# Optimization experiments

Hardware: AMD Instinct MI355X
Metric: run time of the kernel (lower is better)

Reference implementation:

```python
import jax, jax.numpy as jnp
import numpy as np

N_NODES = 50000
N_EDGES = 800000
IN_SIZE, HID_SIZE, OUT_SIZE = 512, 128, 64


def _graph_conv(feat, src, dst, W, b, out_norm, in_norm, activation=None):
    # DGL GraphConv with norm='both': h' = D_in^{-1/2} A D_out^{-1/2} (X W) + b
    x = feat * out_norm[:, None]          # scale by source (out-degree) norm
    x = x @ W                             # dense transform first (in >= out)
    msg = x[src]                          # gather per-edge messages [E, d]
    agg = jax.ops.segment_sum(msg, dst, num_segments=N_NODES)
    h = agg * in_norm[:, None] + b
    if activation is not None:
        h = activation(h)
    return h


def setup_inputs() -> dict:
    key = jax.random.key(0)
    k1, k2, k3, k4, k5, k6, k7 = jax.random.split(key, 7)
    features = jax.random.normal(k1, (N_NODES, IN_SIZE), dtype=jnp.float32)
    src = jax.random.randint(k2, (N_EDGES,), 0, N_NODES, dtype=jnp.int64)
    dst = jax.random.randint(k3, (N_EDGES,), 0, N_NODES, dtype=jnp.int64)
    # Glorot-style init as in dglnn.GraphConv
    W1 = jax.random.normal(k4, (IN_SIZE, HID_SIZE), dtype=jnp.float32) * (1.0 / np.sqrt(IN_SIZE))
    b1 = jnp.zeros((HID_SIZE,), dtype=jnp.float32)
    W2 = jax.random.normal(k5, (HID_SIZE, OUT_SIZE), dtype=jnp.float32) * (1.0 / np.sqrt(HID_SIZE))
    b2 = jnp.zeros((OUT_SIZE,), dtype=jnp.float32)
    return {"features": features, "W1": W1, "b1": b1, "W2": W2, "b2": b2,
            "src": src, "dst": dst}


def reference(features, W1, b1, W2, b2, src, dst):
    ones = jnp.ones((N_EDGES,), dtype=features.dtype)
    out_deg = jax.ops.segment_sum(ones, src, num_segments=N_NODES)
    in_deg = jax.ops.segment_sum(ones, dst, num_segments=N_NODES)
    out_norm = jax.lax.rsqrt(jnp.clip(out_deg, 1.0))  # deg clamped to >=1 as in DGL
    in_norm = jax.lax.rsqrt(jnp.clip(in_deg, 1.0))
    h = _graph_conv(features, src, dst, W1, b1, out_norm, in_norm, activation=jax.nn.relu)
    # dropout omitted (eval mode)
    h = _graph_conv(h, src, dst, W2, b2, out_norm, in_norm, activation=None)
    return h
```

## Files before the change

kernel.cpp:

```cpp
#include <hip/hip_runtime.h>

#define N_NODES 50000
#define IN_SIZE 512
#define HID 128
#define OUT 64
#define NB 256
#define SHIFT 7
#define NBUCK 391
#define NBINS8 12500

typedef _Float16 f16x8 __attribute__((ext_vector_type(8)));
typedef _Float16 f16x4 __attribute__((ext_vector_type(4)));
typedef float    f32x4 __attribute__((ext_vector_type(4)));

__device__ __forceinline__ bool detect_w(const int* p, int t, int* sh) {
    if (t < 64) {
        unsigned long long m = __ballot(p[2 * t + 1] == 0);
        if (t == 0) *sh = (m == ~0ull) ? 1 : 0;
    }
    __syncthreads();
    return *sh != 0;
}

__device__ __forceinline__ int load_idx(const void* p, int e, bool w) {
    return w ? (int)((const long long*)p)[e] : ((const int*)p)[e];
}

__global__ __launch_bounds__(256) void k_hist_wt(const void* __restrict__ srcp,
                                                 const void* __restrict__ dstp,
                                                 int* __restrict__ hist,
                                                 unsigned int* __restrict__ spart,
                                                 int E, int EPB,
                                                 const float* __restrict__ W1, _Float16* __restrict__ W1T,
                                                 const float* __restrict__ W2, _Float16* __restrict__ W2T) {
    const int t = threadIdx.x, b = blockIdx.x;
    if (b >= NB) {
        int i = (b - NB) * 256 + t;
        if (i < IN_SIZE * HID) {
            int k = i >> 7, n = i & (HID - 1);
            W1T[(size_t)n * IN_SIZE + k] = (_Float16)W1[i];
        } else {
            int j = i - IN_SIZE * HID;
            if (j < HID * OUT) {
                int k = j >> 6, n = j & (OUT - 1);
                W2T[(size_t)n * HID + k] = (_Float16)W2[j];
            }
        }
        return;
    }
    __shared__ unsigned int sbins[NBINS8];
    __shared__ int dbins[NBUCK];
    __shared__ int shw;
    for (int i = t; i < NBINS8; i += 256) sbins[i] = 0;
    for (int i = t; i < NBUCK; i += 256) dbins[i] = 0;
    bool w = detect_w((const int*)dstp, t, &shw);
    __syncthreads();
    int eend = min(E, (b + 1) * EPB);
    for (int e = b * EPB + t; e < eend; e += 256) {
        int s = load_idx(srcp, e, w);
        int d = load_idx(dstp, e, w);
        atomicAdd(&dbins[d >> SHIFT], 1);
        atomicAdd(&sbins[s >> 2], 1u << ((s & 3) << 3));
    }
    __syncthreads();
    for (int i = t; i < NBUCK; i += 256) hist[i * NB + b] = dbins[i];
    for (int i = t; i < NBINS8; i += 256) spart[(size_t)b * NBINS8 + i] = sbins[i];
}

__global__ __launch_bounds__(256) void k_scanA(int* __restrict__ hist, int* __restrict__ bsum) {
    __shared__ int s[256];
    const int t = threadIdx.x, g = blockIdx.x;
    int v = hist[g * NB + t];
    s[t] = v;
    __syncthreads();
    for (int off = 1; off < 256; off <<= 1) {
        int u = (t >= off) ? s[t - off] : 0;
        __syncthreads();
        s[t] += u;
        __syncthreads();
    }
    hist[g * NB + t] = s[t] - v;
    if (t == 255) bsum[g] = s[255];
}

__global__ __launch_bounds__(512) void k_scanB(const int* __restrict__ bsum, int* __restrict__ bb) {
    __shared__ int s[512];
    const int t = threadIdx.x;
    int v = (t < NBUCK) ? bsum[t] : 0;
    s[t] = v;
    __syncthreads();
    for (int off = 1; off < 512; off <<= 1) {
        int u = (t >= off) ? s[t - off] : 0;
        __syncthreads();
        s[t] += u;
        __syncthreads();
    }
    if (t <= NBUCK) bb[t] = s[t] - v;
}

__global__ __launch_bounds__(256) void k_cscatter(const void* __restrict__ srcp,
                                                  const void* __restrict__ dstp,
                                                  const int* __restrict__ hist,
                                                  const int* __restrict__ bb,
                                                  unsigned int* __restrict__ tmp,
                                                  int E, int EPB) {
    __shared__ int cur[NBUCK];
    __shared__ int shw;
    const int t = threadIdx.x, b = blockIdx.x;
    for (int i = t; i < NBUCK; i += 256) cur[i] = hist[i * NB + b] + bb[i];
    bool w = detect_w((const int*)dstp, t, &shw);
    __syncthreads();
    int eend = min(E, (b + 1) * EPB);
    for (int e = b * EPB + t; e < eend; e += 256) {
        int s = load_idx(srcp, e, w);
        int d = load_idx(dstp, e, w);
        int pos = atomicAdd(&cur[d >> SHIFT], 1);
        tmp[pos] = (unsigned int)s | ((unsigned int)(d & 127) << 16);
    }
}

__global__ __launch_bounds__(256) void k_fine(const unsigned int* __restrict__ tmp,
                                              const int* __restrict__ bb,
                                              const unsigned int* __restrict__ partial,
                                              int* __restrict__ rp,
                                              int* __restrict__ esrc,
                                              float* __restrict__ innorm,
                                              float* __restrict__ onorm) {
    __shared__ int fcnt[128];
    __shared__ int sc[128];
    __shared__ int fcur[128];
    __shared__ int rs[256][4];
    const int t = threadIdx.x, u = blockIdx.x;
    const int e0 = bb[u], e1 = bb[u + 1];
    if (t < 128) fcnt[t] = 0;
    __syncthreads();
    for (int e = e0 + t; e < e1; e += 256)
        atomicAdd(&fcnt[tmp[e] >> 16], 1);
    {
        const int wrd = t & 31, grp = t >> 5;
        const int wd = u * 32 + wrd;
        int c0 = 0, c1 = 0, c2 = 0, c3 = 0;
        if (wd < NBINS8) {
            for (int b = grp * 32; b < grp * 32 + 32; ++b) {
                unsigned int v = partial[(size_t)b * NBINS8 + wd];
                c0 += (int)(v & 255u);
                c1 += (int)((v >> 8) & 255u);
                c2 += (int)((v >> 16) & 255u);
                c3 += (int)(v >> 24);
            }
        }
        rs[t][0] = c0; rs[t][1] = c1; rs[t][2] = c2; rs[t][3] = c3;
    }
    __syncthreads();
    if (t < 32) {
        const int wd = u * 32 + t;
        if (wd < NBINS8) {
            int d0 = 0, d1 = 0, d2 = 0, d3 = 0;
            for (int g = 0; g < 8; ++g) {
                d0 += rs[g * 32 + t][0]; d1 += rs[g * 32 + t][1];
                d2 += rs[g * 32 + t][2]; d3 += rs[g * 32 + t][3];
            }
            if (d0 < 1) d0 = 1; if (d1 < 1) d1 = 1;
            if (d2 < 1) d2 = 1; if (d3 < 1) d3 = 1;
            int n0 = 4 * wd;
            if (n0     < N_NODES) onorm[n0]     = 1.0f / sqrtf((float)d0);
            if (n0 + 1 < N_NODES) onorm[n0 + 1] = 1.0f / sqrtf((float)d1);
            if (n0 + 2 < N_NODES) onorm[n0 + 2] = 1.0f / sqrtf((float)d2);
            if (n0 + 3 < N_NODES) onorm[n0 + 3] = 1.0f / sqrtf((float)d3);
        }
    }
    if (t < 128) sc[t] = fcnt[t];
    __syncthreads();
    for (int off = 1; off < 128; off <<= 1) {
        int v = (t < 128 && t >= off) ? sc[t - off] : 0;
        __syncthreads();
        if (t < 128) sc[t] += v;
        __syncthreads();
    }
    if (t < 128) {
        int base = e0 + sc[t] - fcnt[t];
        fcur[t] = base;
        int node = u * 128 + t;
        if (node < N_NODES) {
            rp[node] = base;
            int c = fcnt[t]; if (c < 1) c = 1;
            innorm[node] = 1.0f / sqrtf((float)c);
        }
    }
    if (u == NBUCK - 1 && t == 0) rp[N_NODES] = e1;
    __syncthreads();
    for (int e = e0 + t; e < e1; e += 256) {
        unsigned int p = tmp[e];
        int pos = atomicAdd(&fcur[p >> 16], 1);
        esrc[pos] = (int)(p & 0xFFFFu);
    }
}

#define LDA 44
__global__ __launch_bounds__(256) void k_gemm1_mfma(const float* __restrict__ A,
                                                    const _Float16* __restrict__ BT,
                                                    const float* __restrict__ onorm,
                                                    _Float16* __restrict__ X) {
    __shared__ _Float16 As[2][64 * LDA];
    __shared__ _Float16 Bs[2][64 * LDA];
    const int tid  = threadIdx.x;
    const int wave = tid >> 6, lane = tid & 63;
    const int lm = lane & 15, lq = lane >> 4;
    const int row0 = (blockIdx.x >> 1) * 64;
    const int ch   = (blockIdx.x & 1) * 64;

    const int ar = tid >> 2, aq = tid & 3;
    int arow = row0 + ar; if (arow >= N_NODES) arow = N_NODES - 1;
    const float* aptr = A + (size_t)arow * IN_SIZE + aq * 8;
    const int bn = tid >> 2, bq = tid & 3;
    const _Float16* bptr = BT + (size_t)(ch + bn) * IN_SIZE + bq * 8;

    f32x4 acc[4];
#pragma unroll
    for (int nt = 0; nt < 4; ++nt) acc[nt] = (f32x4){0.f, 0.f, 0.f, 0.f};

    {
        float4 a0 = *(const float4*)(aptr);
        float4 a1 = *(const float4*)(aptr + 4);
        f16x8  b0 = *(const f16x8*)(bptr);
        f16x8 ap = {(_Float16)a0.x, (_Float16)a0.y, (_Float16)a0.z, (_Float16)a0.w,
                    (_Float16)a1.x, (_Float16)a1.y, (_Float16)a1.z, (_Float16)a1.w};
        *(f16x8*)&As[0][ar * LDA + aq * 8] = ap;
        *(f16x8*)&Bs[0][bn * LDA + bq * 8] = b0;
    }
    __syncthreads();

#pragma unroll
    for (int kt = 0; kt < IN_SIZE / 32; ++kt) {
        const int k0 = kt * 32;
        const int cur = kt & 1;
        float4 na0, na1; f16x8 nb0;
        const bool more = (k0 + 32) < IN_SIZE;
        if (more) {
            na0 = *(const float4*)(aptr + k0 + 32);
            na1 = *(const float4*)(aptr + k0 + 36);
            nb0 = *(const f16x8*)(bptr + k0 + 32);
        }
        f16x8 af = *(const f16x8*)&As[cur][(wave * 16 + lm) * LDA + lq * 8];
#pragma unroll
        for (int nt = 0; nt < 4; ++nt) {
            f16x8 bf = *(const f16x8*)&Bs[cur][(nt * 16 + lm) * LDA + lq * 8];
            acc[nt] = __builtin_amdgcn_mfma_f32_16x16x32_f16(af, bf, acc[nt], 0, 0, 0);
        }
        if (more) {
            f16x8 ap = {(_Float16)na0.x, (_Float16)na0.y, (_Float16)na0.z, (_Float16)na0.w,
                        (_Float16)na1.x, (_Float16)na1.y, (_Float16)na1.z, (_Float16)na1.w};
            *(f16x8*)&As[cur ^ 1][ar * LDA + aq * 8] = ap;
            *(f16x8*)&Bs[cur ^ 1][bn * LDA + bq * 8] = nb0;
            __syncthreads();
        }
    }
#pragma unroll
    for (int i = 0; i < 4; ++i) {
        int row = row0 + wave * 16 + lq * 4 + i;
        if (row < N_NODES) {
            float on = onorm[row];
            _Float16* o = X + (size_t)row * HID + ch + lm;
#pragma unroll
            for (int nt = 0; nt < 4; ++nt)
                o[nt * 16] = (_Float16)(acc[nt][i] * on);
        }
    }
}

#define LDH 136
__global__ __launch_bounds__(256) void k_agg1_fused(const _Float16* __restrict__ X, const int* __restrict__ rp,
                                                    const int* __restrict__ esrc, const float* __restrict__ innorm,
                                                    const float* __restrict__ onorm, const float* __restrict__ b1,
                                                    const _Float16* __restrict__ W2T, _Float16* __restrict__ X2) {
    __shared__ _Float16 Hs[16 * LDH];
    const int t = threadIdx.x;
    const int ln = t >> 4;
    const int c  = (t & 15) << 3;
    const int n  = blockIdx.x * 16 + ln;
    const int e0 = rp[n], e1 = rp[n + 1];
    float a[8] = {0.f, 0.f, 0.f, 0.f, 0.f, 0.f, 0.f, 0.f};
    int e = e0;
    for (; e + 3 < e1; e += 4) {
        int s0 = esrc[e], s1 = esrc[e + 1], s2 = esrc[e + 2], s3 = esrc[e + 3];
        f16x8 v0 = *(const f16x8*)&X[(size_t)s0 * HID + c];
        f16x8 v1 = *(const f16x8*)&X[(size_t)s1 * HID + c];
        f16x8 v2 = *(const f16x8*)&X[(size_t)s2 * HID + c];
        f16x8 v3 = *(const f16x8*)&X[(size_t)s3 * HID + c];
#pragma unroll
        for (int j = 0; j < 8; ++j)
            a[j] += ((float)v0[j] + (float)v1[j]) + ((float)v2[j] + (float)v3[j]);
    }
    for (; e < e1; ++e) {
        f16x8 v = *(const f16x8*)&X[(size_t)esrc[e] * HID + c];
#pragma unroll
        for (int j = 0; j < 8; ++j) a[j] += (float)v[j];
    }
    const float inn = innorm[n], on = onorm[n];
    float4 bA = *(const float4*)&b1[c];
    float4 bB = *(const float4*)&b1[c + 4];
    const float bv[8] = {bA.x, bA.y, bA.z, bA.w, bB.x, bB.y, bB.z, bB.w};
    f16x8 h;
#pragma unroll
    for (int j = 0; j < 8; ++j)
        h[j] = (_Float16)(fmaxf(a[j] * inn + bv[j], 0.f) * on);
    *(f16x8*)&Hs[ln * LDH + c] = h;
    __syncthreads();

    const int wave = t >> 6, lane = t & 63;
    const int lm = lane & 15, lq = lane >> 4;
    f32x4 acc = (f32x4){0.f, 0.f, 0.f, 0.f};
#pragma unroll
    for (int k0 = 0; k0 < HID; k0 += 32) {
        f16x8 af = *(const f16x8*)&Hs[lm * LDH + k0 + lq * 8];
        f16x8 bf = *(const f16x8*)&W2T[(size_t)(wave * 16 + lm) * HID + k0 + lq * 8];
        acc = __builtin_amdgcn_mfma_f32_16x16x32_f16(af, bf, acc, 0, 0, 0);
    }
    const int n0 = blockIdx.x * 16;
#pragma unroll
    for (int i = 0; i < 4; ++i) {
        int row = n0 + lq * 4 + i;
        X2[(size_t)row * OUT + wave * 16 + lm] = (_Float16)acc[i];
    }
}

__global__ __launch_bounds__(256) void k_agg2(const _Float16* __restrict__ X2, const int* __restrict__ rp,
                                              const int* __restrict__ esrc, const float* __restrict__ innorm,
                                              const float* __restrict__ b2, float* __restrict__ out) {
    const int n = blockIdx.x * 32 + (threadIdx.x >> 3);
    const int c = (threadIdx.x & 7) << 3;
    if (n >= N_NODES) return;
    const int e0 = rp[n], e1 = rp[n + 1];
    float a[8] = {0.f, 0.f, 0.f, 0.f, 0.f, 0.f, 0.f, 0.f};
    int e = e0;
    for (; e + 3 < e1; e += 4) {
        int s0 = esrc[e], s1 = esrc[e + 1], s2 = esrc[e + 2], s3 = esrc[e + 3];
        f16x8 v0 = *(const f16x8*)&X2[(size_t)s0 * OUT + c];
        f16x8 v1 = *(const f16x8*)&X2[(size_t)s1 * OUT + c];
        f16x8 v2 = *(const f16x8*)&X2[(size_t)s2 * OUT + c];
        f16x8 v3 = *(const f16x8*)&X2[(size_t)s3 * OUT + c];
#pragma unroll
        for (int j = 0; j < 8; ++j)
            a[j] += ((float)v0[j] + (float)v1[j]) + ((float)v2[j] + (float)v3[j]);
    }
    for (; e < e1; ++e) {
        f16x8 v = *(const f16x8*)&X2[(size_t)esrc[e] * OUT + c];
#pragma unroll
        for (int j = 0; j < 8; ++j) a[j] += (float)v[j];
    }
    const float inn = innorm[n];
    float4 bA = *(const float4*)&b2[c];
    float4 bB = *(const float4*)&b2[c + 4];
    float* o = out + (size_t)n * OUT + c;
    *(float4*)o       = make_float4(a[0] * inn + bA.x, a[1] * inn + bA.y,
                                    a[2] * inn + bA.z, a[3] * inn + bA.w);
    *(float4*)(o + 4) = make_float4(a[4] * inn + bB.x, a[5] * inn + bB.y,
                                    a[6] * inn + bB.z, a[7] * inn + bB.w);
}

extern "C" void kernel_launch(void* const* d_in, const int* in_sizes, int n_in,
                              void* d_out, int out_size, void* d_ws, size_t ws_size,
                              hipStream_t stream) {
    const float* feat = (const float*)d_in[0];
    const float* W1   = (const float*)d_in[1];
    const float* b1   = (const float*)d_in[2];
    const float* W2   = (const float*)d_in[3];
    const float* b2   = (const float*)d_in[4];
    const void*  srcp = (const void*)d_in[5];
    const void*  dstp = (const void*)d_in[6];
    const int    E    = in_sizes[5];
    float* out = (float*)d_out;

    char* w = (char*)d_ws;
    size_t off = 0;
    auto alloc = [&](size_t bytes) -> void* {
        off = (off + 255) & ~(size_t)255;
        void* p = w + off;
        off += bytes;
        return p;
    };
    int*   hist    = (int*)alloc((size_t)NBUCK * NB * 4);
    int*   bsum    = (int*)alloc((size_t)NBUCK * 4);
    int*   bb      = (int*)alloc((size_t)(NBUCK + 1) * 4);
    int*   rp      = (int*)alloc((size_t)(N_NODES + 1) * 4);
    unsigned int* spart = (unsigned int*)alloc((size_t)NB * NBINS8 * 4);
    unsigned int* tmp   = (unsigned int*)alloc((size_t)E * 4);
    int*   esrc    = (int*)alloc((size_t)E * 4);
    float* onorm   = (float*)alloc((size_t)N_NODES * 4);
    float* innorm  = (float*)alloc((size_t)N_NODES * 4);
    _Float16* W1T  = (_Float16*)alloc((size_t)IN_SIZE * HID * 2);
    _Float16* W2T  = (_Float16*)alloc((size_t)HID * OUT * 2);
    _Float16* X1   = (_Float16*)alloc((size_t)N_NODES * HID * 2);
    _Float16* X2   = (_Float16*)alloc((size_t)N_NODES * OUT * 2);
    (void)ws_size; (void)n_in; (void)out_size;

    const int EPB = (E + NB - 1) / NB;
    const int WTB = (IN_SIZE * HID + HID * OUT + 255) / 256;

    k_hist_wt<<<NB + WTB, 256, 0, stream>>>(srcp, dstp, hist, spart, E, EPB, W1, W1T, W2, W2T);
    k_scanA<<<NBUCK, 256, 0, stream>>>(hist, bsum);
    k_scanB<<<1, 512, 0, stream>>>(bsum, bb);
    k_cscatter<<<NB, 256, 0, stream>>>(srcp, dstp, hist, bb, tmp, E, EPB);
    k_fine<<<NBUCK, 256, 0, stream>>>(tmp, bb, spart, rp, esrc, innorm, onorm);

    k_gemm1_mfma<<<((N_NODES + 63) / 64) * 2, 256, 0, stream>>>(feat, W1T, onorm, X1);
    k_agg1_fused<<<(N_NODES + 15) / 16, 256, 0, stream>>>(X1, rp, esrc, innorm, onorm, b1, W2T, X2);
    k_agg2<<<(N_NODES + 31) / 32, 256, 0, stream>>>(X2, rp, esrc, innorm, b2, out);
}
```

Before: 273.1 us.

## Replace per-block shared out-degree histograms with global atomics; unroll gathers to 8

Out-degree counting moves from per-block packed 8-bit shared-memory histograms (written to a 256x12500 partial buffer and reduced in k_fine) to direct global atomicAdd on a 50000-entry counter, zeroed by a new small kernel. This removes about 12.8 MB of partial writes and reads plus the large shared-memory allocation in the histogram kernel, which should raise its occupancy. In exchange it adds 800K global atomics and an extra launch. Separately, both aggregation kernels unroll the edge gather loop from 4 to 8 to keep more loads in flight.

```diff
diff --git a/kernel.cpp b/kernel.cpp
--- a/kernel.cpp
+++ b/kernel.cpp
@@ -7,7 +7,6 @@
 #define NB 256
 #define SHIFT 7
 #define NBUCK 391
-#define NBINS8 12500
 
 typedef _Float16 f16x8 __attribute__((ext_vector_type(8)));
 typedef _Float16 f16x4 __attribute__((ext_vector_type(4)));
@@ -26,10 +25,15 @@
     return w ? (int)((const long long*)p)[e] : ((const int*)p)[e];
 }
 
+__global__ __launch_bounds__(256) void k_zero(unsigned int* __restrict__ outdeg) {
+    int i = blockIdx.x * 256 + threadIdx.x;
+    if (i < N_NODES) outdeg[i] = 0u;
+}
+
 __global__ __launch_bounds__(256) void k_hist_wt(const void* __restrict__ srcp,
                                                  const void* __restrict__ dstp,
                                                  int* __restrict__ hist,
-                                                 unsigned int* __restrict__ spart,
+                                                 unsigned int* __restrict__ outdeg,
                                                  int E, int EPB,
                                                  const float* __restrict__ W1, _Float16* __restrict__ W1T,
                                                  const float* __restrict__ W2, _Float16* __restrict__ W2T) {
@@ -48,10 +52,8 @@
         }
         return;
     }
-    __shared__ unsigned int sbins[NBINS8];
     __shared__ int dbins[NBUCK];
     __shared__ int shw;
-    for (int i = t; i < NBINS8; i += 256) sbins[i] = 0;
     for (int i = t; i < NBUCK; i += 256) dbins[i] = 0;
     bool w = detect_w((const int*)dstp, t, &shw);
     __syncthreads();
@@ -60,11 +62,10 @@
         int s = load_idx(srcp, e, w);
         int d = load_idx(dstp, e, w);
         atomicAdd(&dbins[d >> SHIFT], 1);
-        atomicAdd(&sbins[s >> 2], 1u << ((s & 3) << 3));
+        atomicAdd(&outdeg[s], 1u);
     }
     __syncthreads();
     for (int i = t; i < NBUCK; i += 256) hist[i * NB + b] = dbins[i];
-    for (int i = t; i < NBINS8; i += 256) spart[(size_t)b * NBINS8 + i] = sbins[i];
 }
 
 __global__ __launch_bounds__(256) void k_scanA(int* __restrict__ hist, int* __restrict__ bsum) {
@@ -121,7 +122,7 @@
 
 __global__ __launch_bounds__(256) void k_fine(const unsigned int* __restrict__ tmp,
                                               const int* __restrict__ bb,
-                                              const unsigned int* __restrict__ partial,
+                                              const unsigned int* __restrict__ outdeg,
                                               int* __restrict__ rp,
                                               int* __restrict__ esrc,
                                               float* __restrict__ innorm,
@@ -129,46 +130,13 @@
     __shared__ int fcnt[128];
     __shared__ int sc[128];
     __shared__ int fcur[128];
-    __shared__ int rs[256][4];
     const int t = threadIdx.x, u = blockIdx.x;
     const int e0 = bb[u], e1 = bb[u + 1];
     if (t < 128) fcnt[t] = 0;
     __syncthreads();
     for (int e = e0 + t; e < e1; e += 256)
         atomicAdd(&fcnt[tmp[e] >> 16], 1);
-    {
-        const int wrd = t & 31, grp = t >> 5;
-        const int wd = u * 32 + wrd;
-        int c0 = 0, c1 = 0, c2 = 0, c3 = 0;
-        if (wd < NBINS8) {
-            for (int b = grp * 32; b < grp * 32 + 32; ++b) {
-                unsigned int v = partial[(size_t)b * NBINS8 + wd];
-                c0 += (int)(v & 255u);
-                c1 += (int)((v >> 8) & 255u);
-                c2 += (int)((v >> 16) & 255u);
-                c3 += (int)(v >> 24);
-            }
-        }
-        rs[t][0] = c0; rs[t][1] = c1; rs[t][2] = c2; rs[t][3] = c3;
-    }
-    __syncthreads();
-    if (t < 32) {
-        const int wd = u * 32 + t;
-        if (wd < NBINS8) {
-            int d0 = 0, d1 = 0, d2 = 0, d3 = 0;
-            for (int g = 0; g < 8; ++g) {
-                d0 += rs[g * 32 + t][0]; d1 += rs[g * 32 + t][1];
-                d2 += rs[g * 32 + t][2]; d3 += rs[g * 32 + t][3];
-            }
-            if (d0 < 1) d0 = 1; if (d1 < 1) d1 = 1;
-            if (d2 < 1) d2 = 1; if (d3 < 1) d3 = 1;
-            int n0 = 4 * wd;
-            if (n0     < N_NODES) onorm[n0]     = 1.0f / sqrtf((float)d0);
-            if (n0 + 1 < N_NODES) onorm[n0 + 1] = 1.0f / sqrtf((float)d1);
-            if (n0 + 2 < N_NODES) onorm[n0 + 2] = 1.0f / sqrtf((float)d2);
-            if (n0 + 3 < N_NODES) onorm[n0 + 3] = 1.0f / sqrtf((float)d3);
-        }
-    }
+    __syncthreads();
     if (t < 128) sc[t] = fcnt[t];
     __syncthreads();
     for (int off = 1; off < 128; off <<= 1) {
@@ -185,6 +153,8 @@
             rp[node] = base;
             int c = fcnt[t]; if (c < 1) c = 1;
             innorm[node] = 1.0f / sqrtf((float)c);
+            unsigned int od = outdeg[node]; if (od < 1u) od = 1u;
+            onorm[node] = 1.0f / sqrtf((float)od);
         }
     }
     if (u == NBUCK - 1 && t == 0) rp[N_NODES] = e1;
@@ -281,15 +251,19 @@
     const int e0 = rp[n], e1 = rp[n + 1];
     float a[8] = {0.f, 0.f, 0.f, 0.f, 0.f, 0.f, 0.f, 0.f};
     int e = e0;
-    for (; e + 3 < e1; e += 4) {
-        int s0 = esrc[e], s1 = esrc[e + 1], s2 = esrc[e + 2], s3 = esrc[e + 3];
-        f16x8 v0 = *(const f16x8*)&X[(size_t)s0 * HID + c];
-        f16x8 v1 = *(const f16x8*)&X[(size_t)s1 * HID + c];
-        f16x8 v2 = *(const f16x8*)&X[(size_t)s2 * HID + c];
-        f16x8 v3 = *(const f16x8*)&X[(size_t)s3 * HID + c];
+    for (; e + 7 < e1; e += 8) {
+        f16x8 v0 = *(const f16x8*)&X[(size_t)esrc[e]     * HID + c];
+        f16x8 v1 = *(const f16x8*)&X[(size_t)esrc[e + 1] * HID + c];
+        f16x8 v2 = *(const f16x8*)&X[(size_t)esrc[e + 2] * HID + c];
+        f16x8 v3 = *(const f16x8*)&X[(size_t)esrc[e + 3] * HID + c];
+        f16x8 v4 = *(const f16x8*)&X[(size_t)esrc[e + 4] * HID + c];
+        f16x8 v5 = *(const f16x8*)&X[(size_t)esrc[e + 5] * HID + c];
+        f16x8 v6 = *(const f16x8*)&X[(size_t)esrc[e + 6] * HID + c];
+        f16x8 v7 = *(const f16x8*)&X[(size_t)esrc[e + 7] * HID + c];
 #pragma unroll
         for (int j = 0; j < 8; ++j)
-            a[j] += ((float)v0[j] + (float)v1[j]) + ((float)v2[j] + (float)v3[j]);
+            a[j] += (((float)v0[j] + (float)v1[j]) + ((float)v2[j] + (float)v3[j])) +
+                    (((float)v4[j] + (float)v5[j]) + ((float)v6[j] + (float)v7[j]));
     }
     for (; e < e1; ++e) {
         f16x8 v = *(const f16x8*)&X[(size_t)esrc[e] * HID + c];
@@ -333,15 +307,19 @@
     const int e0 = rp[n], e1 = rp[n + 1];
     float a[8] = {0.f, 0.f, 0.f, 0.f, 0.f, 0.f, 0.f, 0.f};
     int e = e0;
-    for (; e + 3 < e1; e += 4) {
-        int s0 = esrc[e], s1 = esrc[e + 1], s2 = esrc[e + 2], s3 = esrc[e + 3];
-        f16x8 v0 = *(const f16x8*)&X2[(size_t)s0 * OUT + c];
-        f16x8 v1 = *(const f16x8*)&X2[(size_t)s1 * OUT + c];
-        f16x8 v2 = *(const f16x8*)&X2[(size_t)s2 * OUT + c];
-        f16x8 v3 = *(const f16x8*)&X2[(size_t)s3 * OUT + c];
+    for (; e + 7 < e1; e += 8) {
+        f16x8 v0 = *(const f16x8*)&X2[(size_t)esrc[e]     * OUT + c];
+        f16x8 v1 = *(const f16x8*)&X2[(size_t)esrc[e + 1] * OUT + c];
+        f16x8 v2 = *(const f16x8*)&X2[(size_t)esrc[e + 2] * OUT + c];
+        f16x8 v3 = *(const f16x8*)&X2[(size_t)esrc[e + 3] * OUT + c];
+        f16x8 v4 = *(const f16x8*)&X2[(size_t)esrc[e + 4] * OUT + c];
+        f16x8 v5 = *(const f16x8*)&X2[(size_t)esrc[e + 5] * OUT + c];
+        f16x8 v6 = *(const f16x8*)&X2[(size_t)esrc[e + 6] * OUT + c];
+        f16x8 v7 = *(const f16x8*)&X2[(size_t)esrc[e + 7] * OUT + c];
 #pragma unroll
         for (int j = 0; j < 8; ++j)
-            a[j] += ((float)v0[j] + (float)v1[j]) + ((float)v2[j] + (float)v3[j]);
+            a[j] += (((float)v0[j] + (float)v1[j]) + ((float)v2[j] + (float)v3[j])) +
+                    (((float)v4[j] + (float)v5[j]) + ((float)v6[j] + (float)v7[j]));
     }
     for (; e < e1; ++e) {
         f16x8 v = *(const f16x8*)&X2[(size_t)esrc[e] * OUT + c];
@@ -383,7 +361,7 @@
     int*   bsum    = (int*)alloc((size_t)NBUCK * 4);
     int*   bb      = (int*)alloc((size_t)(NBUCK + 1) * 4);
     int*   rp      = (int*)alloc((size_t)(N_NODES + 1) * 4);
-    unsigned int* spart = (unsigned int*)alloc((size_t)NB * NBINS8 * 4);
+    unsigned int* outdeg = (unsigned int*)alloc((size_t)N_NODES * 4);
     unsigned int* tmp   = (unsigned int*)alloc((size_t)E * 4);
     int*   esrc    = (int*)alloc((size_t)E * 4);
     float* onorm   = (float*)alloc((size_t)N_NODES * 4);
@@ -396,12 +374,14 @@
 
     const int EPB = (E + NB - 1) / NB;
     const int WTB = (IN_SIZE * HID + HID * OUT + 255) / 256;
-
-    k_hist_wt<<<NB + WTB, 256, 0, stream>>>(srcp, dstp, hist, spart, E, EPB, W1, W1T, W2, W2T);
+    const int ZB  = (N_NODES + 255) / 256;
+
+    k_zero<<<ZB, 256, 0, stream>>>(outdeg);
+    k_hist_wt<<<NB + WTB, 256, 0, stream>>>(srcp, dstp, hist, outdeg, E, EPB, W1, W1T, W2, W2T);
     k_scanA<<<NBUCK, 256, 0, stream>>>(hist, bsum);
     k_scanB<<<1, 512, 0, stream>>>(bsum, bb);
     k_cscatter<<<NB, 256, 0, stream>>>(srcp, dstp, hist, bb, tmp, E, EPB);
-    k_fine<<<NBUCK, 256, 0, stream>>>(tmp, bb, spart, rp, esrc, innorm, onorm);
+    k_fine<<<NBUCK, 256, 0, stream>>>(tmp, bb, outdeg, rp, esrc, innorm, onorm);
 
     k_gemm1_mfma<<<((N_NODES + 63) / 64) * 2, 256, 0, stream>>>(feat, W1T, onorm, X1);
     k_agg1_fused<<<(N_NODES + 15) / 16, 256, 0, stream>>>(X1, rp, esrc, innorm, onorm, b1, W2T, X2);
```

Result: slower. 299.3 us (+9.6%).

## Fuse CSR-construction kernels into one cooperative kernel with grid syncs

Applied to the files above, without the earlier changes.

Replaces the five separate kernels that build the CSR (histogram plus weight transpose, two-level scan, coarse scatter, fine sort and norms) with a single cooperative kernel of NBUCK blocks. The phases are separated by grid-wide syncs instead of kernel boundaries. The weight transpose now runs in the spare blocks with a strided loop. This is meant to remove launch overhead and inter-kernel gaps. In exchange it adds grid-barrier cost, uses a large shared-memory footprint per block that limits occupancy, and depends on all blocks being co-resident.

```diff
diff --git a/kernel.cpp b/kernel.cpp
--- a/kernel.cpp
+++ b/kernel.cpp
@@ -1,4 +1,7 @@
 #include <hip/hip_runtime.h>
+#include <hip/hip_cooperative_groups.h>
+
+namespace cg = cooperative_groups;
 
 #define N_NODES 50000
 #define IN_SIZE 512
@@ -26,173 +29,168 @@
     return w ? (int)((const long long*)p)[e] : ((const int*)p)[e];
 }
 
-__global__ __launch_bounds__(256) void k_hist_wt(const void* __restrict__ srcp,
-                                                 const void* __restrict__ dstp,
-                                                 int* __restrict__ hist,
-                                                 unsigned int* __restrict__ spart,
-                                                 int E, int EPB,
-                                                 const float* __restrict__ W1, _Float16* __restrict__ W1T,
-                                                 const float* __restrict__ W2, _Float16* __restrict__ W2T) {
+__global__ __launch_bounds__(256) void k_csr_coop(const void* __restrict__ srcp,
+                                                  const void* __restrict__ dstp,
+                                                  int* __restrict__ hist,
+                                                  unsigned int* __restrict__ spart,
+                                                  int E, int EPB,
+                                                  const float* __restrict__ W1, _Float16* __restrict__ W1T,
+                                                  const float* __restrict__ W2, _Float16* __restrict__ W2T,
+                                                  int* __restrict__ bsum, int* __restrict__ bb,
+                                                  int* __restrict__ rp, unsigned int* __restrict__ tmp,
+                                                  int* __restrict__ esrc,
+                                                  float* __restrict__ innorm, float* __restrict__ onorm) {
+    cg::grid_group grid = cg::this_grid();
+    __shared__ unsigned int sbins[NBINS8];
+    __shared__ int dbins[NBUCK];
+    __shared__ int shw;
+    __shared__ int s1[256];
+    __shared__ int ping[512], pong[512];
+    __shared__ int fcnt[128], sc[128], fcur[128];
+    __shared__ int rs[256][4];
     const int t = threadIdx.x, b = blockIdx.x;
-    if (b >= NB) {
-        int i = (b - NB) * 256 + t;
-        if (i < IN_SIZE * HID) {
-            int k = i >> 7, n = i & (HID - 1);
-            W1T[(size_t)n * IN_SIZE + k] = (_Float16)W1[i];
-        } else {
-            int j = i - IN_SIZE * HID;
-            if (j < HID * OUT) {
+    bool w = false;
+
+    if (b < NB) {
+        for (int i = t; i < NBINS8; i += 256) sbins[i] = 0;
+        for (int i = t; i < NBUCK; i += 256) dbins[i] = 0;
+        w = detect_w((const int*)dstp, t, &shw);
+        __syncthreads();
+        int eend = min(E, (b + 1) * EPB);
+        for (int e = b * EPB + t; e < eend; e += 256) {
+            int s = load_idx(srcp, e, w);
+            int d = load_idx(dstp, e, w);
+            atomicAdd(&dbins[d >> SHIFT], 1);
+            atomicAdd(&sbins[s >> 2], 1u << ((s & 3) << 3));
+        }
+        __syncthreads();
+        for (int i = t; i < NBUCK; i += 256) hist[i * NB + b] = dbins[i];
+        for (int i = t; i < NBINS8; i += 256) spart[(size_t)b * NBINS8 + i] = sbins[i];
+    } else {
+        const int total = IN_SIZE * HID + HID * OUT;
+        for (int i = (b - NB) * 256 + t; i < total; i += (NBUCK - NB) * 256) {
+            if (i < IN_SIZE * HID) {
+                int k = i >> 7, n = i & (HID - 1);
+                W1T[(size_t)n * IN_SIZE + k] = (_Float16)W1[i];
+            } else {
+                int j = i - IN_SIZE * HID;
                 int k = j >> 6, n = j & (OUT - 1);
                 W2T[(size_t)n * HID + k] = (_Float16)W2[j];
             }
         }
-        return;
-    }
-    __shared__ unsigned int sbins[NBINS8];
-    __shared__ int dbins[NBUCK];
-    __shared__ int shw;
-    for (int i = t; i < NBINS8; i += 256) sbins[i] = 0;
-    for (int i = t; i < NBUCK; i += 256) dbins[i] = 0;
-    bool w = detect_w((const int*)dstp, t, &shw);
-    __syncthreads();
-    int eend = min(E, (b + 1) * EPB);
-    for (int e = b * EPB + t; e < eend; e += 256) {
-        int s = load_idx(srcp, e, w);
-        int d = load_idx(dstp, e, w);
-        atomicAdd(&dbins[d >> SHIFT], 1);
-        atomicAdd(&sbins[s >> 2], 1u << ((s & 3) << 3));
-    }
-    __syncthreads();
-    for (int i = t; i < NBUCK; i += 256) hist[i * NB + b] = dbins[i];
-    for (int i = t; i < NBINS8; i += 256) spart[(size_t)b * NBINS8 + i] = sbins[i];
-}
-
-__global__ __launch_bounds__(256) void k_scanA(int* __restrict__ hist, int* __restrict__ bsum) {
-    __shared__ int s[256];
-    const int t = threadIdx.x, g = blockIdx.x;
-    int v = hist[g * NB + t];
-    s[t] = v;
-    __syncthreads();
-    for (int off = 1; off < 256; off <<= 1) {
-        int u = (t >= off) ? s[t - off] : 0;
-        __syncthreads();
-        s[t] += u;
-        __syncthreads();
-    }
-    hist[g * NB + t] = s[t] - v;
-    if (t == 255) bsum[g] = s[255];
-}
-
-__global__ __launch_bounds__(512) void k_scanB(const int* __restrict__ bsum, int* __restrict__ bb) {
-    __shared__ int s[512];
-    const int t = threadIdx.x;
-    int v = (t < NBUCK) ? bsum[t] : 0;
-    s[t] = v;
-    __syncthreads();
-    for (int off = 1; off < 512; off <<= 1) {
-        int u = (t >= off) ? s[t - off] : 0;
-        __syncthreads();
-        s[t] += u;
-        __syncthreads();
-    }
-    if (t <= NBUCK) bb[t] = s[t] - v;
-}
-
-__global__ __launch_bounds__(256) void k_cscatter(const void* __restrict__ srcp,
-                                                  const void* __restrict__ dstp,
-                                                  const int* __restrict__ hist,
-                                                  const int* __restrict__ bb,
-                                                  unsigned int* __restrict__ tmp,
-                                                  int E, int EPB) {
-    __shared__ int cur[NBUCK];
-    __shared__ int shw;
-    const int t = threadIdx.x, b = blockIdx.x;
-    for (int i = t; i < NBUCK; i += 256) cur[i] = hist[i * NB + b] + bb[i];
-    bool w = detect_w((const int*)dstp, t, &shw);
-    __syncthreads();
-    int eend = min(E, (b + 1) * EPB);
-    for (int e = b * EPB + t; e < eend; e += 256) {
-        int s = load_idx(srcp, e, w);
-        int d = load_idx(dstp, e, w);
-        int pos = atomicAdd(&cur[d >> SHIFT], 1);
-        tmp[pos] = (unsigned int)s | ((unsigned int)(d & 127) << 16);
-    }
-}
-
-__global__ __launch_bounds__(256) void k_fine(const unsigned int* __restrict__ tmp,
-                                              const int* __restrict__ bb,
-                                              const unsigned int* __restrict__ partial,
-                                              int* __restrict__ rp,
-                                              int* __restrict__ esrc,
-                                              float* __restrict__ innorm,
-                                              float* __restrict__ onorm) {
-    __shared__ int fcnt[128];
-    __shared__ int sc[128];
-    __shared__ int fcur[128];
-    __shared__ int rs[256][4];
-    const int t = threadIdx.x, u = blockIdx.x;
-    const int e0 = bb[u], e1 = bb[u + 1];
-    if (t < 128) fcnt[t] = 0;
-    __syncthreads();
-    for (int e = e0 + t; e < e1; e += 256)
-        atomicAdd(&fcnt[tmp[e] >> 16], 1);
+    }
+    grid.sync();
+
     {
-        const int wrd = t & 31, grp = t >> 5;
-        const int wd = u * 32 + wrd;
-        int c0 = 0, c1 = 0, c2 = 0, c3 = 0;
-        if (wd < NBINS8) {
-            for (int b = grp * 32; b < grp * 32 + 32; ++b) {
-                unsigned int v = partial[(size_t)b * NBINS8 + wd];
-                c0 += (int)(v & 255u);
-                c1 += (int)((v >> 8) & 255u);
-                c2 += (int)((v >> 16) & 255u);
-                c3 += (int)(v >> 24);
+        int v = hist[b * NB + t];
+        s1[t] = v;
+        __syncthreads();
+        for (int off = 1; off < 256; off <<= 1) {
+            int u = (t >= off) ? s1[t - off] : 0;
+            __syncthreads();
+            s1[t] += u;
+            __syncthreads();
+        }
+        hist[b * NB + t] = s1[t] - v;
+        if (t == 255) bsum[b] = s1[255];
+    }
+    grid.sync();
+
+    if (b == 0) {
+        int v0 = (t < NBUCK) ? bsum[t] : 0;
+        int v1 = (t + 256 < NBUCK) ? bsum[t + 256] : 0;
+        ping[t] = v0; ping[t + 256] = v1;
+        __syncthreads();
+        int* sB = ping; int* dB = pong;
+        for (int off = 1; off < 512; off <<= 1) {
+            dB[t]       = sB[t]       + ((t >= off) ? sB[t - off] : 0);
+            dB[t + 256] = sB[t + 256] + ((t + 256 >= off) ? sB[t + 256 - off] : 0);
+            __syncthreads();
+            int* tp = sB; sB = dB; dB = tp;
+        }
+        if (t <= NBUCK) bb[t] = sB[t] - v0;
+        if (t + 256 <= NBUCK) bb[t + 256] = sB[t + 256] - v1;
+    }
+    grid.sync();
+
+    if (b < NB) {
+        for (int i = t; i < NBUCK; i += 256) dbins[i] = hist[i * NB + b] + bb[i];
+        __syncthreads();
+        int eend = min(E, (b + 1) * EPB);
+        for (int e = b * EPB + t; e < eend; e += 256) {
+            int s = load_idx(srcp, e, w);
+            int d = load_idx(dstp, e, w);
+            int pos = atomicAdd(&dbins[d >> SHIFT], 1);
+            tmp[pos] = (unsigned int)s | ((unsigned int)(d & 127) << 16);
+        }
+    }
+    grid.sync();
+
+    {
+        const int u = b;
+        const int e0 = bb[u], e1 = bb[u + 1];
+        if (t < 128) fcnt[t] = 0;
+        __syncthreads();
+        for (int e = e0 + t; e < e1; e += 256)
+            atomicAdd(&fcnt[tmp[e] >> 16], 1);
+        {
+            const int wrd = t & 31, grp = t >> 5;
+            const int wd = u * 32 + wrd;
+            int c0 = 0, c1 = 0, c2 = 0, c3 = 0;
+            if (wd < NBINS8) {
+                for (int p = grp * 32; p < grp * 32 + 32; ++p) {
+                    unsigned int v = spart[(size_t)p * NBINS8 + wd];
+                    c0 += (int)(v & 255u);
+                    c1 += (int)((v >> 8) & 255u);
+                    c2 += (int)((v >> 16) & 255u);
+                    c3 += (int)(v >> 24);
+                }
             }
-        }
-        rs[t][0] = c0; rs[t][1] = c1; rs[t][2] = c2; rs[t][3] = c3;
-    }
-    __syncthreads();
-    if (t < 32) {
-        const int wd = u * 32 + t;
-        if (wd < NBINS8) {
-            int d0 = 0, d1 = 0, d2 = 0, d3 = 0;
-            for (int g = 0; g < 8; ++g) {
-                d0 += rs[g * 32 + t][0]; d1 += rs[g * 32 + t][1];
-                d2 += rs[g * 32 + t][2]; d3 += rs[g * 32 + t][3];
+            rs[t][0] = c0; rs[t][1] = c1; rs[t][2] = c2; rs[t][3] = c3;
+        }
+        __syncthreads();
+        if (t < 32) {
+            const int wd = u * 32 + t;
+            if (wd < NBINS8) {
+                int d0 = 0, d1 = 0, d2 = 0, d3 = 0;
+                for (int g = 0; g < 8; ++g) {
+                    d0 += rs[g * 32 + t][0]; d1 += rs[g * 32 + t][1];
+                    d2 += rs[g * 32 + t][2]; d3 += rs[g * 32 + t][3];
+                }
+                if (d0 < 1) d0 = 1; if (d1 < 1) d1 = 1;
+                if (d2 < 1) d2 = 1; if (d3 < 1) d3 = 1;
+                int n0 = 4 * wd;
+                if (n0     < N_NODES) onorm[n0]     = 1.0f / sqrtf((float)d0);
+                if (n0 + 1 < N_NODES) onorm[n0 + 1] = 1.0f / sqrtf((float)d1);
+                if (n0 + 2 < N_NODES) onorm[n0 + 2] = 1.0f / sqrtf((float)d2);
+                if (n0 + 3 < N_NODES) onorm[n0 + 3] = 1.0f / sqrtf((float)d3);
             }
-            if (d0 < 1) d0 = 1; if (d1 < 1) d1 = 1;
-            if (d2 < 1) d2 = 1; if (d3 < 1) d3 = 1;
-            int n0 = 4 * wd;
-            if (n0     < N_NODES) onorm[n0]     = 1.0f / sqrtf((float)d0);
-            if (n0 + 1 < N_NODES) onorm[n0 + 1] = 1.0f / sqrtf((float)d1);
-            if (n0 + 2 < N_NODES) onorm[n0 + 2] = 1.0f / sqrtf((float)d2);
-            if (n0 + 3 < N_NODES) onorm[n0 + 3] = 1.0f / sqrtf((float)d3);
-        }
-    }
-    if (t < 128) sc[t] = fcnt[t];
-    __syncthreads();
-    for (int off = 1; off < 128; off <<= 1) {
-        int v = (t < 128 && t >= off) ? sc[t - off] : 0;
-        __syncthreads();
-        if (t < 128) sc[t] += v;
-        __syncthreads();
-    }
-    if (t < 128) {
-        int base = e0 + sc[t] - fcnt[t];
-        fcur[t] = base;
-        int node = u * 128 + t;
-        if (node < N_NODES) {
-            rp[node] = base;
-            int c = fcnt[t]; if (c < 1) c = 1;
-            innorm[node] = 1.0f / sqrtf((float)c);
-        }
-    }
-    if (u == NBUCK - 1 && t == 0) rp[N_NODES] = e1;
-    __syncthreads();
-    for (int e = e0 + t; e < e1; e += 256) {
-        unsigned int p = tmp[e];
-        int pos = atomicAdd(&fcur[p >> 16], 1);
-        esrc[pos] = (int)(p & 0xFFFFu);
+        }
+        if (t < 128) sc[t] = fcnt[t];
+        __syncthreads();
+        for (int off = 1; off < 128; off <<= 1) {
+            int v = (t < 128 && t >= off) ? sc[t - off] : 0;
+            __syncthreads();
+            if (t < 128) sc[t] += v;
+            __syncthreads();
+        }
+        if (t < 128) {
+            int base = e0 + sc[t] - fcnt[t];
+            fcur[t] = base;
+            int node = u * 128 + t;
+            if (node < N_NODES) {
+                rp[node] = base;
+                int c = fcnt[t]; if (c < 1) c = 1;
+                innorm[node] = 1.0f / sqrtf((float)c);
+            }
+        }
+        if (u == NBUCK - 1 && t == 0) rp[N_NODES] = e1;
+        __syncthreads();
+        for (int e = e0 + t; e < e1; e += 256) {
+            unsigned int p = tmp[e];
+            int pos = atomicAdd(&fcur[p >> 16], 1);
+            esrc[pos] = (int)(p & 0xFFFFu);
+        }
     }
 }
 
@@ -394,14 +392,16 @@
     _Float16* X2   = (_Float16*)alloc((size_t)N_NODES * OUT * 2);
     (void)ws_size; (void)n_in; (void)out_size;
 
-    const int EPB = (E + NB - 1) / NB;
-    const int WTB = (IN_SIZE * HID + HID * OUT + 255) / 256;
-
-    k_hist_wt<<<NB + WTB, 256, 0, stream>>>(srcp, dstp, hist, spart, E, EPB, W1, W1T, W2, W2T);
-    k_scanA<<<NBUCK, 256, 0, stream>>>(hist, bsum);
-    k_scanB<<<1, 512, 0, stream>>>(bsum, bb);
-    k_cscatter<<<NB, 256, 0, stream>>>(srcp, dstp, hist, bb, tmp, E, EPB);
-    k_fine<<<NBUCK, 256, 0, stream>>>(tmp, bb, spart, rp, esrc, innorm, onorm);
+    int EPB = (E + NB - 1) / NB;
+    int Ev  = E;
+
+    void* cargs[] = {(void*)&srcp, (void*)&dstp, (void*)&hist, (void*)&spart,
+                     (void*)&Ev, (void*)&EPB,
+                     (void*)&W1, (void*)&W1T, (void*)&W2, (void*)&W2T,
+                     (void*)&bsum, (void*)&bb, (void*)&rp, (void*)&tmp, (void*)&esrc,
+                     (void*)&innorm, (void*)&onorm};
+    hipLaunchCooperativeKernel((const void*)k_csr_coop, dim3(NBUCK), dim3(256),
+                               cargs, 0, stream);
 
     k_gemm1_mfma<<<((N_NODES + 63) / 64) * 2, 256, 0, stream>>>(feat, W1T, onorm, X1);
     k_agg1_fused<<<(N_NODES + 15) / 16, 256, 0, stream>>>(X1, rp, esrc, innorm, onorm, b1, W2T, X2);
```

Measured after the change: 479.4 us. +75.5%, slower.
